# Kernel optimization log

Measured on AMD Instinct MI355X. Metric: run time of the kernel, lower is better.

## Reference

```python
import jax, jax.numpy as jnp
import numpy as np
import math

H = 12  # num heads
EPS = 1e-5


def layer_norm(x, g, b):
    xf = x.astype(jnp.float32)
    mu = jnp.mean(xf, axis=-1, keepdims=True)
    var = jnp.var(xf, axis=-1, keepdims=True)
    return ((xf - mu) * jax.lax.rsqrt(var + EPS) * g + b).astype(x.dtype)


def setup_inputs() -> dict:
    key = jax.random.key(0)
    ks = jax.random.split(key, 8)
    C, M = 768, 3072
    s = 0.02
    inp = {
        "x": jax.random.normal(ks[0], (128, 197, C), dtype=jnp.float32),
        # linear weights stored as [in, out] (y = x @ W + b)
        "Wq": jax.random.normal(ks[1], (C, C), dtype=jnp.float32) * s,
        "bq": jnp.zeros((C,), jnp.float32),
        "Wk": jax.random.normal(ks[2], (C, C), dtype=jnp.float32) * s,
        "bk": jnp.zeros((C,), jnp.float32),
        "Wv": jax.random.normal(ks[3], (C, C), dtype=jnp.float32) * s,
        "bv": jnp.zeros((C,), jnp.float32),
        "Wo": jax.random.normal(ks[4], (C, C), dtype=jnp.float32) * s,
        "bo": jnp.zeros((C,), jnp.float32),
        "W1": jax.random.normal(ks[5], (C, M), dtype=jnp.float32) * s,
        "b1": jnp.zeros((M,), jnp.float32),
        "W2": jax.random.normal(ks[6], (M, C), dtype=jnp.float32) * s,
        "b2": jnp.zeros((C,), jnp.float32),
        "g1": jnp.ones((C,), jnp.float32),
        "beta1": jnp.zeros((C,), jnp.float32),
        "g2": jnp.ones((C,), jnp.float32),
        "beta2": jnp.zeros((C,), jnp.float32),
    }
    return inp


def attention(xn, Wq, bq, Wk, bk, Wv, bv, Wo, bo):
    N, L, C = xn.shape
    Cqk = C // H
    q = (xn @ Wq + bq).reshape(N, L, H, Cqk)
    k = (xn @ Wk + bk).reshape(N, L, H, Cqk)
    v = (xn @ Wv + bv).reshape(N, L, H, Cqk)
    scale = 1.0 / math.sqrt(Cqk)
    aff = jnp.einsum('nqhc,nkhc->nqkh', q * scale, k)  # [N, Lq, Lk, H]
    aff = jax.nn.softmax(aff, axis=-2)                  # softmax over key axis
    mix = jnp.einsum('nqlh,nlhc->nqhc', aff, v)
    return mix.reshape(N, L, C) @ Wo + bo


def reference(x, Wq, bq, Wk, bk, Wv, bv, Wo, bo, W1, b1, W2, b2, g1, beta1, g2, beta2):
    x = x + attention(layer_norm(x, g1, beta1), Wq, bq, Wk, bk, Wv, bv, Wo, bo)
    h = layer_norm(x, g2, beta2) @ W1 + b1
    h = h * jax.nn.sigmoid(1.702 * h)  # QuickGELU
    return x + h @ W2 + b2
```

## Files before the change

kernel.cpp:

```cpp
#include <hip/hip_runtime.h>
#include <hip/hip_bf16.h>

typedef __bf16 bf16_t;
typedef __bf16 bf16x8 __attribute__((ext_vector_type(8)));
typedef float f32x4 __attribute__((ext_vector_type(4)));

#define T_TOK 25216
#define C_DIM 768
#define NH 12
#define LSEQ 197

__device__ __forceinline__ void gload_lds16(const bf16_t* g, bf16_t* l) {
  __builtin_amdgcn_global_load_lds(
      (const __attribute__((address_space(1))) unsigned int*)g,
      (__attribute__((address_space(3))) unsigned int*)l, 16, 0, 0);
}

__global__ void wtrans_k(const float* __restrict__ W, bf16_t* __restrict__ Wt,
                         int K, int N) {
  __shared__ float tile[32][33];
  const int tx = threadIdx.x, ty = threadIdx.y;
  const int bx = blockIdx.x, by = blockIdx.y;
#pragma unroll
  for (int i = ty; i < 32; i += 8)
    tile[i][tx] = W[(long)(by * 32 + i) * N + bx * 32 + tx];
  __syncthreads();
#pragma unroll
  for (int i = ty; i < 32; i += 8)
    Wt[(long)(bx * 32 + i) * K + by * 32 + tx] = (bf16_t)tile[tx][i];
}

__global__ void cat3_k(const float* __restrict__ a, const float* __restrict__ b,
                       const float* __restrict__ c, float* __restrict__ o) {
  int i = blockIdx.x * 256 + threadIdx.x;
  if (i < 2304) o[i] = i < 768 ? a[i] : (i < 1536 ? b[i - 768] : c[i - 1536]);
}

__global__ __launch_bounds__(256) void ln_k(const float* __restrict__ x,
                                            const float* __restrict__ g,
                                            const float* __restrict__ b,
                                            bf16_t* __restrict__ o) {
  const int lane = threadIdx.x & 63;
  const long row = (long)blockIdx.x * 4 + (threadIdx.x >> 6);
  const float* xr = x + row * C_DIM;
  float4 v[3];
  float s = 0.f, sq = 0.f;
#pragma unroll
  for (int i = 0; i < 3; ++i) {
    v[i] = *(const float4*)&xr[i * 256 + lane * 4];
    s += v[i].x + v[i].y + v[i].z + v[i].w;
    sq += v[i].x * v[i].x + v[i].y * v[i].y + v[i].z * v[i].z + v[i].w * v[i].w;
  }
#pragma unroll
  for (int off = 32; off; off >>= 1) {
    s += __shfl_xor(s, off);
    sq += __shfl_xor(sq, off);
  }
  const float mu = s * (1.f / 768.f);
  const float rstd = rsqrtf(sq * (1.f / 768.f) - mu * mu + 1e-5f);
  bf16_t* orow = o + row * C_DIM;
#pragma unroll
  for (int i = 0; i < 3; ++i) {
    const int c = i * 256 + lane * 4;
    const float4 gg = *(const float4*)&g[c];
    const float4 bb = *(const float4*)&b[c];
    bf16_t t4[4];
    t4[0] = (bf16_t)((v[i].x - mu) * rstd * gg.x + bb.x);
    t4[1] = (bf16_t)((v[i].y - mu) * rstd * gg.y + bb.y);
    t4[2] = (bf16_t)((v[i].z - mu) * rstd * gg.z + bb.z);
    t4[3] = (bf16_t)((v[i].w - mu) * rstd * gg.w + bb.w);
    __builtin_memcpy(&orow[c], t4, 8);
  }
}

template <int EPI, int BM, int BN>
__global__ __launch_bounds__(256) void gemm_bt(
    const bf16_t* __restrict__ A, const bf16_t* __restrict__ Bt,
    const float* __restrict__ bias, const float* __restrict__ res,
    void* __restrict__ outp, int K, int N) {
  constexpr int MACC = BM / 32;
  constexpr int NACC = BN / 32;
  constexpr int ACW = BM / 32;
  constexpr int BCW = BN / 32;
  __shared__ __align__(16) bf16_t lA[BM * 64];
  __shared__ __align__(16) bf16_t lB[BN * 64];
  const int tid = threadIdx.x;
  const int wave = tid >> 6, lane = tid & 63;
  const int fr = lane & 15, fq = lane >> 4;

  const int gx = gridDim.x;
  const int nwg = gridDim.x * gridDim.y;
  int bid = blockIdx.y * gx + blockIdx.x;
  {
    const int q = nwg >> 3, r = nwg & 7;
    const int xcd = bid & 7, idx = bid >> 3;
    bid = (xcd < r ? xcd * (q + 1) : r * (q + 1) + (xcd - r) * q) + idx;
  }
  const int bx = bid % gx, by = bid / gx;

  const long rowBase = (long)by * BM;
  const long colBase = (long)bx * BN;
  const int wr = (wave >> 1) * (BM / 2), wc = (wave & 1) * (BN / 2);

  f32x4 acc[MACC][NACC];
#pragma unroll
  for (int m = 0; m < MACC; ++m)
#pragma unroll
    for (int n = 0; n < NACC; ++n) acc[m][n] = (f32x4){0.f, 0.f, 0.f, 0.f};

  const int srow = lane >> 3;
  const int scol = (((lane & 7) ^ srow)) * 8;
  const int kTiles = K >> 6;
  for (int kt = 0; kt < kTiles; ++kt) {
    const long k0 = (long)kt * 64;
#pragma unroll
    for (int c = 0; c < ACW; ++c) {
      const int g = wave * ACW + c;
      gload_lds16(A + (rowBase + 8 * g + srow) * K + k0 + scol, lA + g * 512);
    }
#pragma unroll
    for (int c = 0; c < BCW; ++c) {
      const int g = wave * BCW + c;
      gload_lds16(Bt + (colBase + 8 * g + srow) * K + k0 + scol, lB + g * 512);
    }
    __syncthreads();
#pragma unroll
    for (int kf = 0; kf < 2; ++kf) {
      bf16x8 af[MACC], bfr[NACC];
#pragma unroll
      for (int m = 0; m < MACC; ++m) {
        const int row = wr + m * 16 + fr;
        af[m] = *(const bf16x8*)&lA[row * 64 + (((kf * 4 + fq) ^ (fr & 7)) * 8)];
      }
#pragma unroll
      for (int n = 0; n < NACC; ++n) {
        const int row = wc + n * 16 + fr;
        bfr[n] = *(const bf16x8*)&lB[row * 64 + (((kf * 4 + fq) ^ (fr & 7)) * 8)];
      }
#pragma unroll
      for (int m = 0; m < MACC; ++m)
#pragma unroll
        for (int n = 0; n < NACC; ++n)
          acc[m][n] = __builtin_amdgcn_mfma_f32_16x16x32_bf16(af[m], bfr[n],
                                                              acc[m][n], 0, 0, 0);
    }
    __syncthreads();
  }

#pragma unroll
  for (int m = 0; m < MACC; ++m) {
    const long row0 = rowBase + wr + m * 16 + fq * 4;
#pragma unroll
    for (int n = 0; n < NACC; ++n) {
      const long col = colBase + wc + n * 16 + fr;
      const float bb = bias[col];
#pragma unroll
      for (int r = 0; r < 4; ++r) {
        const long idx = (row0 + r) * N + col;
        float v = acc[m][n][r] + bb;
        if (EPI == 0) {
          ((bf16_t*)outp)[idx] = (bf16_t)v;
        } else if (EPI == 1) {
          ((float*)outp)[idx] = v + res[idx];
        } else {
          v = v / (1.f + __expf(-1.702f * v));
          ((bf16_t*)outp)[idx] = (bf16_t)v;
        }
      }
    }
  }
}

__global__ __launch_bounds__(256) void attn_k(const bf16_t* __restrict__ qkv,
                                              bf16_t* __restrict__ mix) {
  constexpr int KR = 72;
  constexpr int VR = 232;
  __shared__ __align__(16) bf16_t smem[208 * KR + 64 * VR + 64 * VR];
  bf16_t* lK = smem;
  bf16_t* lVt = smem + 208 * KR;
  bf16_t* lP = lVt + 64 * VR;

  const int tid = threadIdx.x;
  const int wave = tid >> 6, lane = tid & 63;
  const int fr = lane & 15, fq = lane >> 4;
  const int nh = blockIdx.x;
  const int n = nh / NH, h = nh % NH;
  const long t0 = (long)n * LSEQ;
  const long qs = 2304;

  {
    int4 z = {0, 0, 0, 0};
    int4* p = (int4*)smem;
    const int tot = (208 * KR + 2 * 64 * VR) * 2 / 16;
    for (int i = tid; i < tot; i += 256) p[i] = z;
  }
  __syncthreads();

  for (int it = tid; it < 197 * 8; it += 256) {
    int r = it >> 3, cg = it & 7;
    int4 v = *(const int4*)(qkv + (t0 + r) * qs + 768 + h * 64 + cg * 8);
    *(int4*)&lK[r * KR + cg * 8] = v;
  }
  for (int it = tid; it < 197 * 8; it += 256) {
    int r = it >> 3, cg = it & 7;
    int4 v = *(const int4*)(qkv + (t0 + r) * qs + 1536 + h * 64 + cg * 8);
    const bf16_t* pv = (const bf16_t*)&v;
#pragma unroll
    for (int j = 0; j < 8; ++j) lVt[(cg * 8 + j) * VR + r] = pv[j];
  }
  __syncthreads();

  bf16_t* lPw = lP + wave * 16 * VR;

  for (int fi = 0; fi < 4; ++fi) {
    const int f = wave + fi * 4;
    if (f >= 13) break;
    const int qrow = f * 16 + fr;
    const long tq = t0 + (qrow < LSEQ ? qrow : LSEQ - 1);
    const bf16_t* qp = qkv + tq * qs + h * 64;
    bf16x8 a0 = *(const bf16x8*)(qp + fq * 8);
    bf16x8 a1 = *(const bf16x8*)(qp + 32 + fq * 8);

    f32x4 s[13];
#pragma unroll
    for (int j = 0; j < 13; ++j) s[j] = (f32x4){0.f, 0.f, 0.f, 0.f};
#pragma unroll
    for (int j = 0; j < 13; ++j) {
      bf16x8 b0 = *(const bf16x8*)&lK[(j * 16 + fr) * KR + fq * 8];
      s[j] = __builtin_amdgcn_mfma_f32_16x16x32_bf16(a0, b0, s[j], 0, 0, 0);
      bf16x8 b1 = *(const bf16x8*)&lK[(j * 16 + fr) * KR + 32 + fq * 8];
      s[j] = __builtin_amdgcn_mfma_f32_16x16x32_bf16(a1, b1, s[j], 0, 0, 0);
    }
    float mx[4] = {-3e38f, -3e38f, -3e38f, -3e38f};
#pragma unroll
    for (int j = 0; j < 13; ++j) {
      const bool valid = (j * 16 + fr) < LSEQ;
#pragma unroll
      for (int r = 0; r < 4; ++r) {
        float v = s[j][r] * 0.125f;
        v = valid ? v : -3e38f;
        s[j][r] = v;
        mx[r] = fmaxf(mx[r], v);
      }
    }
#pragma unroll
    for (int r = 0; r < 4; ++r) {
      mx[r] = fmaxf(mx[r], __shfl_xor(mx[r], 1));
      mx[r] = fmaxf(mx[r], __shfl_xor(mx[r], 2));
      mx[r] = fmaxf(mx[r], __shfl_xor(mx[r], 4));
      mx[r] = fmaxf(mx[r], __shfl_xor(mx[r], 8));
    }
    float sm[4] = {0.f, 0.f, 0.f, 0.f};
#pragma unroll
    for (int j = 0; j < 13; ++j)
#pragma unroll
      for (int r = 0; r < 4; ++r) {
        float e = __expf(s[j][r] - mx[r]);
        s[j][r] = e;
        sm[r] += e;
      }
#pragma unroll
    for (int r = 0; r < 4; ++r) {
      sm[r] += __shfl_xor(sm[r], 1);
      sm[r] += __shfl_xor(sm[r], 2);
      sm[r] += __shfl_xor(sm[r], 4);
      sm[r] += __shfl_xor(sm[r], 8);
      sm[r] = 1.f / sm[r];
    }
#pragma unroll
    for (int j = 0; j < 13; ++j)
#pragma unroll
      for (int r = 0; r < 4; ++r)
        lPw[(fq * 4 + r) * VR + j * 16 + fr] = (bf16_t)(s[j][r] * sm[r]);
    asm volatile("s_waitcnt lgkmcnt(0)" ::: "memory");

    f32x4 o4[4];
#pragma unroll
    for (int c = 0; c < 4; ++c) o4[c] = (f32x4){0.f, 0.f, 0.f, 0.f};
#pragma unroll
    for (int kc = 0; kc < 7; ++kc) {
      bf16x8 pa = *(const bf16x8*)&lPw[fr * VR + kc * 32 + fq * 8];
#pragma unroll
      for (int c = 0; c < 4; ++c) {
        bf16x8 bv = *(const bf16x8*)&lVt[(c * 16 + fr) * VR + kc * 32 + fq * 8];
        o4[c] = __builtin_amdgcn_mfma_f32_16x16x32_bf16(pa, bv, o4[c], 0, 0, 0);
      }
    }
#pragma unroll
    for (int c = 0; c < 4; ++c)
#pragma unroll
      for (int r = 0; r < 4; ++r) {
        const int q = f * 16 + fq * 4 + r;
        if (q < LSEQ)
          mix[(t0 + q) * C_DIM + h * 64 + c * 16 + fr] = (bf16_t)o4[c][r];
      }
  }
}

extern "C" void kernel_launch(void* const* d_in, const int* in_sizes, int n_in,
                              void* d_out, int out_size, void* d_ws,
                              size_t ws_size, hipStream_t stream) {
  const float* x = (const float*)d_in[0];
  const float* Wq = (const float*)d_in[1];
  const float* bq = (const float*)d_in[2];
  const float* Wk = (const float*)d_in[3];
  const float* bk = (const float*)d_in[4];
  const float* Wv = (const float*)d_in[5];
  const float* bv = (const float*)d_in[6];
  const float* Wo = (const float*)d_in[7];
  const float* bo = (const float*)d_in[8];
  const float* W1 = (const float*)d_in[9];
  const float* b1 = (const float*)d_in[10];
  const float* W2 = (const float*)d_in[11];
  const float* b2 = (const float*)d_in[12];
  const float* g1 = (const float*)d_in[13];
  const float* be1 = (const float*)d_in[14];
  const float* g2 = (const float*)d_in[15];
  const float* be2 = (const float*)d_in[16];

  char* ws = (char*)d_ws;
  size_t off = 0;
  auto alloc = [&](size_t bytes) {
    char* p = ws + off;
    off += (bytes + 255) & ~(size_t)255;
    return p;
  };
  bf16_t* xn = (bf16_t*)alloc((size_t)T_TOK * 768 * 2);
  char* qm = alloc((size_t)T_TOK * 3072 * 2);
  bf16_t* qkv = (bf16_t*)qm;
  bf16_t* mixb = (bf16_t*)(qm + (size_t)T_TOK * 2304 * 2);
  bf16_t* h = (bf16_t*)qm;
  bf16_t* Wqkvt = (bf16_t*)alloc((size_t)2304 * 768 * 2);
  bf16_t* Wot = (bf16_t*)alloc((size_t)768 * 768 * 2);
  bf16_t* W1t = (bf16_t*)alloc((size_t)3072 * 768 * 2);
  bf16_t* W2t = (bf16_t*)alloc((size_t)768 * 3072 * 2);
  float* bqkv = (float*)alloc(2304 * 4);
  float* x2 = (float*)d_out;

  dim3 tb(32, 8);
  wtrans_k<<<dim3(24, 24), tb, 0, stream>>>(Wq, Wqkvt, 768, 768);
  wtrans_k<<<dim3(24, 24), tb, 0, stream>>>(Wk, Wqkvt + 768 * 768, 768, 768);
  wtrans_k<<<dim3(24, 24), tb, 0, stream>>>(Wv, Wqkvt + 2 * 768 * 768, 768, 768);
  wtrans_k<<<dim3(24, 24), tb, 0, stream>>>(Wo, Wot, 768, 768);
  wtrans_k<<<dim3(96, 24), tb, 0, stream>>>(W1, W1t, 768, 3072);
  wtrans_k<<<dim3(24, 96), tb, 0, stream>>>(W2, W2t, 3072, 768);
  cat3_k<<<9, 256, 0, stream>>>(bq, bk, bv, bqkv);

  ln_k<<<T_TOK / 4, 256, 0, stream>>>(x, g1, be1, xn);
  gemm_bt<0, 128, 128><<<dim3(2304 / 128, T_TOK / 128), 256, 0, stream>>>(
      xn, Wqkvt, bqkv, nullptr, qkv, 768, 2304);
  attn_k<<<128 * NH, 256, 0, stream>>>(qkv, mixb);
  gemm_bt<1, 64, 128><<<dim3(768 / 128, T_TOK / 64), 256, 0, stream>>>(
      mixb, Wot, bo, x, x2, 768, 768);
  ln_k<<<T_TOK / 4, 256, 0, stream>>>(x2, g2, be2, xn);
  gemm_bt<2, 128, 128><<<dim3(3072 / 128, T_TOK / 128), 256, 0, stream>>>(
      xn, W1t, b1, nullptr, h, 768, 3072);
  gemm_bt<1, 64, 128><<<dim3(768 / 128, T_TOK / 64), 256, 0, stream>>>(
      h, W2t, b2, x2, (float*)d_out, 3072, 768);
}
```

Measured before the change: 758.7 us.

## Double-buffer LDS tiles in GEMM to overlap global loads with MFMA

Replaces the single-buffered load-sync-compute loop in the bf16 GEMM with a two-stage ping-pong LDS pipeline. The next K tile is loaded asynchronously via global_load_lds while the current tile is computed, using explicit vmcnt waits and barriers. Base pointers are precomputed to cut address arithmetic. LDS use doubles, which can lower occupancy, and the tail logic assumes an even number of K tiles (true for K=768 and 3072).

```diff
diff --git a/kernel.cpp b/kernel.cpp
--- a/kernel.cpp
+++ b/kernel.cpp
@@ -14,6 +14,17 @@
   __builtin_amdgcn_global_load_lds(
       (const __attribute__((address_space(1))) unsigned int*)g,
       (__attribute__((address_space(3))) unsigned int*)l, 16, 0, 0);
+}
+
+template <int N>
+__device__ __forceinline__ void vm_wait() {
+  asm volatile("s_waitcnt vmcnt(%0)" ::"n"(N) : "memory");
+}
+__device__ __forceinline__ void block_bar() {
+  __builtin_amdgcn_sched_barrier(0);
+  asm volatile("" ::: "memory");
+  __builtin_amdgcn_s_barrier();
+  __builtin_amdgcn_sched_barrier(0);
 }
 
 __global__ void wtrans_k(const float* __restrict__ W, bf16_t* __restrict__ Wt,
@@ -82,8 +93,9 @@
   constexpr int NACC = BN / 32;
   constexpr int ACW = BM / 32;
   constexpr int BCW = BN / 32;
-  __shared__ __align__(16) bf16_t lA[BM * 64];
-  __shared__ __align__(16) bf16_t lB[BN * 64];
+  constexpr int NLOADS = ACW + BCW;
+  __shared__ __align__(16) bf16_t lA[2][BM * 64];
+  __shared__ __align__(16) bf16_t lB[2][BN * 64];
   const int tid = threadIdx.x;
   const int wave = tid >> 6, lane = tid & 63;
   const int fr = lane & 15, fq = lane >> 4;
@@ -110,32 +122,47 @@
 
   const int srow = lane >> 3;
   const int scol = (((lane & 7) ^ srow)) * 8;
-  const int kTiles = K >> 6;
-  for (int kt = 0; kt < kTiles; ++kt) {
-    const long k0 = (long)kt * 64;
-#pragma unroll
-    for (int c = 0; c < ACW; ++c) {
-      const int g = wave * ACW + c;
-      gload_lds16(A + (rowBase + 8 * g + srow) * K + k0 + scol, lA + g * 512);
-    }
-#pragma unroll
-    for (int c = 0; c < BCW; ++c) {
-      const int g = wave * BCW + c;
-      gload_lds16(Bt + (colBase + 8 * g + srow) * K + k0 + scol, lB + g * 512);
-    }
-    __syncthreads();
+
+  const bf16_t* aP[ACW];
+  const bf16_t* bP[BCW];
+#pragma unroll
+  for (int c = 0; c < ACW; ++c)
+    aP[c] = A + (rowBase + 8 * (wave * ACW + c) + srow) * (long)K + scol;
+#pragma unroll
+  for (int c = 0; c < BCW; ++c)
+    bP[c] = Bt + (colBase + 8 * (wave * BCW + c) + srow) * (long)K + scol;
+
+  auto stage0 = [&](int koff) {
+#pragma unroll
+    for (int c = 0; c < ACW; ++c)
+      gload_lds16(aP[c] + koff, &lA[0][(wave * ACW + c) * 512]);
+#pragma unroll
+    for (int c = 0; c < BCW; ++c)
+      gload_lds16(bP[c] + koff, &lB[0][(wave * BCW + c) * 512]);
+  };
+  auto stage1 = [&](int koff) {
+#pragma unroll
+    for (int c = 0; c < ACW; ++c)
+      gload_lds16(aP[c] + koff, &lA[1][(wave * ACW + c) * 512]);
+#pragma unroll
+    for (int c = 0; c < BCW; ++c)
+      gload_lds16(bP[c] + koff, &lB[1][(wave * BCW + c) * 512]);
+  };
+  auto compute0 = [&]() {
 #pragma unroll
     for (int kf = 0; kf < 2; ++kf) {
       bf16x8 af[MACC], bfr[NACC];
 #pragma unroll
       for (int m = 0; m < MACC; ++m) {
         const int row = wr + m * 16 + fr;
-        af[m] = *(const bf16x8*)&lA[row * 64 + (((kf * 4 + fq) ^ (fr & 7)) * 8)];
+        af[m] =
+            *(const bf16x8*)&lA[0][row * 64 + (((kf * 4 + fq) ^ (fr & 7)) * 8)];
       }
 #pragma unroll
       for (int n = 0; n < NACC; ++n) {
         const int row = wc + n * 16 + fr;
-        bfr[n] = *(const bf16x8*)&lB[row * 64 + (((kf * 4 + fq) ^ (fr & 7)) * 8)];
+        bfr[n] =
+            *(const bf16x8*)&lB[0][row * 64 + (((kf * 4 + fq) ^ (fr & 7)) * 8)];
       }
 #pragma unroll
       for (int m = 0; m < MACC; ++m)
@@ -144,8 +171,54 @@
           acc[m][n] = __builtin_amdgcn_mfma_f32_16x16x32_bf16(af[m], bfr[n],
                                                               acc[m][n], 0, 0, 0);
     }
-    __syncthreads();
-  }
+  };
+  auto compute1 = [&]() {
+#pragma unroll
+    for (int kf = 0; kf < 2; ++kf) {
+      bf16x8 af[MACC], bfr[NACC];
+#pragma unroll
+      for (int m = 0; m < MACC; ++m) {
+        const int row = wr + m * 16 + fr;
+        af[m] =
+            *(const bf16x8*)&lA[1][row * 64 + (((kf * 4 + fq) ^ (fr & 7)) * 8)];
+      }
+#pragma unroll
+      for (int n = 0; n < NACC; ++n) {
+        const int row = wc + n * 16 + fr;
+        bfr[n] =
+            *(const bf16x8*)&lB[1][row * 64 + (((kf * 4 + fq) ^ (fr & 7)) * 8)];
+      }
+#pragma unroll
+      for (int m = 0; m < MACC; ++m)
+#pragma unroll
+        for (int n = 0; n < NACC; ++n)
+          acc[m][n] = __builtin_amdgcn_mfma_f32_16x16x32_bf16(af[m], bfr[n],
+                                                              acc[m][n], 0, 0, 0);
+    }
+  };
+
+  const int kT = K >> 6;
+  stage0(0);
+  int kt = 0;
+  for (; kt + 2 < kT; kt += 2) {
+    stage1((kt + 1) * 64);
+    vm_wait<NLOADS>();
+    block_bar();
+    compute0();
+    block_bar();
+    stage0((kt + 2) * 64);
+    vm_wait<NLOADS>();
+    block_bar();
+    compute1();
+    block_bar();
+  }
+  stage1((kt + 1) * 64);
+  vm_wait<NLOADS>();
+  block_bar();
+  compute0();
+  vm_wait<0>();
+  block_bar();
+  compute1();
 
 #pragma unroll
   for (int m = 0; m < MACC; ++m) {
```

New measurement: 724.5 us. -4.5%, faster.
